# Kernel optimization log

Hardware: AMD Instinct MI355X
Metric: run time of the kernel (lower is better)

Reference implementation:

```python
import jax, jax.numpy as jnp
import numpy as np

B, T = 4096, 2048
CLIP = 1.0e5


def _hv(x):
    # smooth Heaviside: ~0 for x<0, ~1 for x>0
    return (jnp.tanh(5.0 * x) + 1.0) * 0.5


def setup_inputs() -> dict:
    key = jax.random.key(0)
    k1, _ = jax.random.split(key)
    # columns: prcp, tmean, dayl (all in [0,1) like normalized forcings)
    inputs = jax.random.uniform(k1, (B, T, 3), dtype=jnp.float32)
    # 15 scalar bucket parameters, all initialized to 0.5 as in build():
    # f, smax, qmax, ddf, tmin, tmax, Kc, SCmax, spmax, qpmax, kp, sgmax, qgmax, Kl, Kn
    theta = jnp.full((15,), 0.5, dtype=jnp.float32)
    return {"inputs": inputs, "theta": theta}


def _run(inputs, theta):
    f, smax, qmax, ddf, tmin, tmax, Kc, SCmax, spmax, qpmax, kp, sgmax, qgmax, Kl, Kn = [
        theta[i] for i in range(15)
    ]
    prcp = inputs[:, :, 0]   # [B,T]
    tmean = inputs[:, :, 1]
    dayl = inputs[:, :, 2]
    # Hamon-style PET computed once for the whole sequence
    pet = 29.8 * (dayl * 24.0) * 0.611 * jnp.exp(17.3 * tmean / (tmean + 237.3)) / (tmean + 273.2)

    # rescaled parameters (done once; constant over time)
    f_ = f / 10.0
    smax_ = smax * 1950.0
    qmax_ = qmax * 50.0
    ddf_ = ddf * 5.0
    tmin_ = tmin * -3.0
    tmax_ = tmax * 3.0
    Kc_ = Kc * 0.5
    SCmax_ = SCmax * 1.5
    spmax_ = spmax * 1950.0
    qpmax_ = qpmax * 40.0
    sgmax_ = sgmax * 1950.0
    qgmax_ = qgmax * 40.0
    Kl_ = Kl * 0.5
    Kn_ = Kn * 0.5
    Dc = 0.986 * 0.862

    def step(state, xt):
        s0, s1, s2, s3, s4 = [state[:, i] for i in range(5)]  # each [B]
        p, t, dl, pe = xt  # each [B]

        # canopy bucket
        day = _hv(dl - 0.5)
        night = _hv(0.5 - dl)
        scmax_t = day * SCmax_ * 2.0 + night * SCmax_ * 0.6
        lai_t = day * 0.478 + night * 0.15
        kc_t = day * Kc_ + night * Kc_ * 0.4
        pintc = (_hv(p - 0.1) * _hv(s0) * _hv(s0 - scmax_t) * p
                 + _hv(p - 0.1) * _hv(scmax_t - s0) * kc_t * Dc * lai_t)

        # rain/snow partition
        psnow = _hv(tmin_ - t) * p
        prain = _hv(t - tmin_) * p

        # snow bucket
        melt = _hv(t - tmax_) * _hv(s1) * jnp.minimum(s1, ddf_ * (t - tmax_))

        # preferential bucket
        qpref = (_hv(s2) * _hv(s2 - spmax_) * qpmax_
                 + _hv(s2) * _hv(spmax_ - s2) * kp * p * jnp.exp(-f_ * (spmax_ - s2)))

        # capillary (soil) bucket
        et = (_hv(s3) * _hv(s3 - smax_) * pe
              + _hv(s3) * _hv(smax_ - s3) * pe * (s3 / smax_))
        qsub = (_hv(s3) * _hv(s3 - smax_) * qmax_
                + _hv(s3) * _hv(smax_ - s3) * qmax_ * jnp.exp(-f_ * (smax_ - s3)))
        qout = _hv(s3) * _hv(s3 - smax_) * (s3 - smax_)

        # gravity bucket
        qslow = (_hv(s4) * _hv(s4 - sgmax_) * qgmax_
                 + _hv(s4) * _hv(sgmax_ - s4) * (p * Kl_ + p * p * Kn_) * jnp.exp(-f_ * (sgmax_ - s4)))

        ns0 = s0 + jnp.clip(pintc, -CLIP, CLIP)
        ns1 = s1 + jnp.clip(psnow - melt, -CLIP, CLIP)
        ns2 = s2 + jnp.clip(qpref, -CLIP, CLIP)
        ns3 = s3 + jnp.clip(prain + melt - et - qsub - qout, -CLIP, CLIP)
        ns4 = s4 + jnp.clip(qslow, -CLIP, CLIP)
        new_state = jnp.stack([ns0, ns1, ns2, ns3, ns4], axis=1)  # [B,5]
        return new_state, new_state

    init = jnp.zeros((inputs.shape[0], 5), dtype=inputs.dtype)
    xs = (prcp.T, tmean.T, dayl.T, pet.T)  # time-major [T,B]
    _, seq = jax.lax.scan(step, init, xs)  # seq: [T,B,5]
    return jnp.transpose(seq, (1, 0, 2))  # [B,T,5] state trajectories


def reference(inputs, theta):
    return _run(inputs, theta)
```

## Files before the change

kernel.cpp:

```cpp
#include <hip/hip_runtime.h>


#define NB 4096
#define NT 2048
#define CH0 16
#define K1 16
#define CH23 32
#define BT ((size_t)NB * (size_t)NT)

#define L2E10 14.4269504089f
#define L2E    1.44269504089f

__device__ __forceinline__ float rcpf(float x) { return __builtin_amdgcn_rcpf(x); }
__device__ __forceinline__ float ex2(float a)  { return __builtin_amdgcn_exp2f(a); }
__device__ __forceinline__ float ex2c(float a) { return __builtin_amdgcn_exp2f(fminf(a, 80.0f)); }
__device__ __forceinline__ float clip1e5(float x) {
    return __builtin_amdgcn_fmed3f(x, -100000.0f, 100000.0f);
}
__device__ __forceinline__ void pinbuf(const float* d, int n4) {
    const float4* v = (const float4*)d;
    #pragma unroll
    for (int i = 0; i < n4; ++i)
        asm volatile("" :: "v"(v[i].x), "v"(v[i].y), "v"(v[i].z), "v"(v[i].w));
}

__global__ __launch_bounds__(256)
void pre_kernel(const float* __restrict__ inp, const float* __restrict__ theta,
                float* __restrict__ out, float* __restrict__ wsp, int use_p0) {
    const float ddf_   = theta[3] * 5.0f;
    const float tmin_  = theta[4] * -3.0f;
    const float tmax_  = theta[5] * 3.0f;
    const float Kc_    = theta[6] * 0.5f;
    const float SCmax_ = theta[7] * 1.5f;
    const float KcDc  = Kc_ * 0.849932f;
    const float c_sn  = -L2E10 * tmin_;
    const float c_m   =  L2E10 * tmax_;
    const float c_dd  = -ddf_ * tmax_;
    const float c_sc1 =  L2E10 * SCmax_ * 1.4f;
    const float c_sc0 =  L2E10 * SCmax_ * 0.6f;

    const size_t k = (size_t)blockIdx.x * 256 + threadIdx.x;
    const float4* i4 = (const float4*)(inp + k * 12);
    const float4 A = i4[0], Bv = i4[1], C = i4[2];
    const float P[4] = {A.x, A.w, Bv.z, C.y};
    const float T[4] = {A.y, Bv.x, Bv.w, C.z};
    const float D[4] = {A.z, Bv.y, C.x, C.w};

    float4 pk1[4], pk0[4];
    float pp[4];
    #pragma unroll
    for (int j = 0; j < 4; ++j) {
        const float p = P[j], tm = T[j], dl = D[j];
        const float A1 = tm + 237.3f;
        const float A2 = tm + 273.2f;
        const float q  = rcpf(A1 * A2);
        const float pe = 436.98672f * dl * ex2(24.958624f * tm * (q * A2)) * (q * A1);
        const float psnow = rcpf(1.0f + ex2(fmaf(L2E10, tm, c_sn))) * p;
        const float dm  = 1.0f + ex2(fmaf(-L2E10, tm, c_m));
        const float mdd = fmaf(ddf_, tm, c_dd);
        pk1[j] = make_float4(pe, psnow, dm, mdd);
        pp[j] = p;
        if (use_p0) {
            const float day = rcpf(1.0f + ex2(fmaf(-L2E10, dl, 7.21347520f)));
            const float da  = 1.0f + ex2(fmaf(-L2E10, p, L2E));
            const float lai   = fmaf(0.328f, day, 0.15f);
            const float kcf   = fmaf(0.6f, day, 0.4f);
            const float kterm = KcDc * kcf * lai;
            const float zday  = fmaf(c_sc1, day, c_sc0);
            pk0[j] = make_float4(p, kterm, zday, da);
        }
    }
    float4* o1 = (float4*)out + k * 4;
    #pragma unroll
    for (int j = 0; j < 4; ++j) o1[j] = pk1[j];
    *(float4*)(out + 4 * BT + k * 4) = make_float4(pp[0], pp[1], pp[2], pp[3]);
    if (use_p0) {
        float4* o0 = (float4*)(wsp + 5 * BT) + k * 4;
        #pragma unroll
        for (int j = 0; j < 4; ++j) o0[j] = pk0[j];
    }
}

__global__ __launch_bounds__(64, 1)
void prnn_roles(const float* __restrict__ inp, const float* __restrict__ theta,
                float* __restrict__ out, float* __restrict__ wsp,
                int use_ws, int use_p0) {
    const int lane = threadIdx.x;
    const int role = blockIdx.x & 3;
    const int b = (blockIdx.x >> 2) * 64 + lane;

    const float f_     = theta[0] * 0.1f;
    const float smax_  = theta[1] * 1950.0f;
    const float qmax_  = theta[2] * 50.0f;
    const float ddf_   = theta[3] * 5.0f;
    const float tmin_  = theta[4] * -3.0f;
    const float tmax_  = theta[5] * 3.0f;
    const float Kc_    = theta[6] * 0.5f;
    const float SCmax_ = theta[7] * 1.5f;
    const float spmax_ = theta[8] * 1950.0f;
    const float qpmax_ = theta[9] * 40.0f;
    const float kp     = theta[10];
    const float sgmax_ = theta[11] * 1950.0f;
    const float qgmax_ = theta[12] * 40.0f;
    const float Kl_    = theta[13] * 0.5f;
    const float Kn_    = theta[14] * 0.5f;

    const float inv_smax = rcpf(smax_);
    const float KcDc  = Kc_ * 0.849932f;
    const float c_sn  = -L2E10 * tmin_;
    const float c_m   =  L2E10 * tmax_;
    const float c_dd  = -ddf_ * tmax_;
    const float c_sc1 =  L2E10 * SCmax_ * 1.4f;
    const float c_sc0 =  L2E10 * SCmax_ * 0.6f;
    const float c_2p  =  L2E10 * spmax_;
    const float c_3s  =  L2E10 * smax_;
    const float c_4s  =  L2E10 * sgmax_;
    const float fE    = f_ * L2E;
    const float c_E2  = -fE * spmax_;
    const float c_E3  = -fE * smax_;
    const float c_E4  = -fE * sgmax_;

    const float* ip = inp + (size_t)b * (NT * 3);
    float*       op = out + (size_t)b * (NT * 5);
    float* wbase = use_ws ? wsp : out;

    auto plane_storeN = [&](float* plane, const float* ob, int off, int n4) {
        float4* d = (float4*)(plane + (size_t)off);
        const float4* s = (const float4*)ob;
        #pragma unroll
        for (int i = 0; i < 8; ++i) { if (i < n4) d[i] = s[i]; }
    };

    if (role == 0) {
        float s0 = 0.f;
        float* w0 = wbase + 0 * BT + (size_t)b * NT;
        if (use_ws && use_p0) {
            const float4* PK = (const float4*)(wsp + 5 * BT) + (size_t)b * NT;
            float bA[CH0 * 4], bB[CH0 * 4];
            auto pf = [&](float* d, int c) {
                #pragma unroll
                for (int i = 0; i < CH0; ++i)
                    ((float4*)d)[i] = PK[(size_t)c * CH0 + i];
            };
            auto cw = [&](const float* d, int c) {
                float ob[CH0];
                #pragma unroll
                for (int i = 0; i < CH0; ++i) {
                    const float p     = d[i * 4 + 0];
                    const float kterm = d[i * 4 + 1];
                    const float zday  = d[i * 4 + 2];
                    const float da    = d[i * 4 + 3];
                    const float e0  = ex2(-L2E10 * s0);
                    const float esc = ex2(fmaf(-L2E10, s0, zday));
                    const float d0  = 1.0f + e0;
                    const float dsc = 1.0f + esc;
                    const float Rp  = rcpf(da * d0 * dsc);
                    const float pintc = Rp * fmaf(d0 * esc, kterm, p);
                    s0 += clip1e5(pintc);
                    ob[i] = s0;
                }
                plane_storeN(w0, ob, c * CH0, CH0 / 4);
            };
            pf(bA, 0);
            for (int c = 0; c < NT / CH0; c += 2) {
                pf(bB, c + 1);
                pinbuf(bA, CH0);
                cw(bA, c);
                if (c + 2 < NT / CH0) pf(bA, c + 2);
                pinbuf(bB, CH0);
                cw(bB, c + 1);
            }
        } else {
            float bA[CH0 * 3], bB[CH0 * 3];
            auto pf = [&](float* d, int c) {
                const float4* s = (const float4*)(ip + (size_t)c * (CH0 * 3));
                #pragma unroll
                for (int i = 0; i < (CH0 * 3) / 4; ++i) ((float4*)d)[i] = s[i];
            };
            auto cw = [&](const float* d, int c) {
                float ob[CH0];
                #pragma unroll
                for (int i = 0; i < CH0; ++i) {
                    const float p  = d[i * 3 + 0];
                    const float dl = d[i * 3 + 2];
                    const float day = rcpf(1.0f + ex2(fmaf(-L2E10, dl, 7.21347520f)));
                    const float da  = 1.0f + ex2(fmaf(-L2E10, p, L2E));
                    const float lai   = fmaf(0.328f, day, 0.15f);
                    const float kcf   = fmaf(0.6f, day, 0.4f);
                    const float kterm = KcDc * kcf * lai;
                    const float zday  = fmaf(c_sc1, day, c_sc0);
                    const float e0  = ex2(-L2E10 * s0);
                    const float esc = ex2(fmaf(-L2E10, s0, zday));
                    const float d0  = 1.0f + e0;
                    const float dsc = 1.0f + esc;
                    const float Rp  = rcpf(da * d0 * dsc);
                    const float pintc = Rp * fmaf(d0 * esc, kterm, p);
                    s0 += clip1e5(pintc);
                    ob[i] = s0;
                }
                if (use_ws) plane_storeN(w0, ob, c * CH0, CH0 / 4);
                else {
                    #pragma unroll
                    for (int i = 0; i < CH0; ++i) op[(c * CH0 + i) * 5 + 0] = ob[i];
                }
            };
            pf(bA, 0);
            for (int c = 0; c < NT / CH0; c += 2) {
                pf(bB, c + 1);
                pinbuf(bA, (CH0 * 3) / 4);
                cw(bA, c);
                if (c + 2 < NT / CH0) pf(bA, c + 2);
                pinbuf(bB, (CH0 * 3) / 4);
                cw(bB, c + 1);
            }
        }
    } else if (role == 1) {
        float s1 = 0.f, s3 = 0.f;
        float* w1 = wbase + 1 * BT + (size_t)b * NT;
        float* w3 = wbase + 3 * BT + (size_t)b * NT;
        if (use_ws) {
            const float4* PK = (const float4*)out + (size_t)b * NT;
            const float*  PP = out + 4 * BT + (size_t)b * NT;
            float kA[K1 * 4], kB[K1 * 4], pA[K1], pB[K1];
            float ob1[2 * K1], ob3[2 * K1];
            auto pf = [&](float* kd, float* pd, int c) {
                #pragma unroll
                for (int i = 0; i < K1; ++i)
                    ((float4*)kd)[i] = PK[(size_t)c * K1 + i];
                #pragma unroll
                for (int i = 0; i < K1 / 4; ++i)
                    ((float4*)pd)[i] = *(const float4*)(PP + (size_t)c * K1 + i * 4);
            };
            auto cw = [&](const float* kd, const float* pd, int half) {
                #pragma unroll
                for (int i = 0; i < K1; ++i) {
                    const float pe    = kd[i * 4 + 0];
                    const float psnow = kd[i * 4 + 1];
                    const float dm    = kd[i * 4 + 2];
                    const float mdd   = kd[i * 4 + 3];
                    const float prain = pd[i] - psnow;
                    const float e1 = ex2(-L2E10 * s1);
                    const float melt = rcpf(dm * (1.0f + e1)) * fminf(s1, mdd);
                    const float e3  = ex2(-L2E10 * s3);
                    const float e3s = ex2c(fmaf(-L2E10, s3, c_3s));
                    const float R3  = rcpf((1.0f + e3) * (1.0f + e3s));
                    const float E3  = ex2(fmaf(fE, s3, c_E3));
                    const float t_et = pe * fmaf(e3s * s3, inv_smax, 1.0f);
                    const float t_qs = qmax_ * fmaf(e3s, E3, 1.0f);
                    const float outflux = R3 * (t_et + t_qs + (s3 - smax_));
                    const float ds3 = prain + melt - outflux;
                    s1 += clip1e5(psnow - melt);
                    s3 += clip1e5(ds3);
                    ob1[half * K1 + i] = s1;
                    ob3[half * K1 + i] = s3;
                }
            };
            pf(kA, pA, 0);
            for (int c = 0; c < NT / K1; c += 2) {
                pf(kB, pB, c + 1);
                pinbuf(kA, K1); pinbuf(pA, K1 / 4);
                cw(kA, pA, 0);
                if (c + 2 < NT / K1) pf(kA, pA, c + 2);
                pinbuf(kB, K1); pinbuf(pB, K1 / 4);
                cw(kB, pB, 1);
                plane_storeN(w1, ob1, c * K1, (2 * K1) / 4);
                plane_storeN(w3, ob3, c * K1, (2 * K1) / 4);
            }
        } else {
            float bA[CH0 * 3], bB[CH0 * 3];
            auto pf = [&](float* d, int c) {
                const float4* s = (const float4*)(ip + (size_t)c * (CH0 * 3));
                #pragma unroll
                for (int i = 0; i < (CH0 * 3) / 4; ++i) ((float4*)d)[i] = s[i];
            };
            auto cw = [&](const float* d, int c) {
                #pragma unroll
                for (int i = 0; i < CH0; ++i) {
                    const float p  = d[i * 3 + 0];
                    const float tm = d[i * 3 + 1];
                    const float dl = d[i * 3 + 2];
                    const float A1 = tm + 237.3f;
                    const float A2 = tm + 273.2f;
                    const float qq = rcpf(A1 * A2);
                    const float pe = 436.98672f * dl * ex2(24.958624f * tm * (qq * A2)) * (qq * A1);
                    const float psnow = rcpf(1.0f + ex2(fmaf(L2E10, tm, c_sn))) * p;
                    const float dm = 1.0f + ex2(fmaf(-L2E10, tm, c_m));
                    const float prain = p - psnow;
                    const float e1 = ex2(-L2E10 * s1);
                    const float melt = rcpf(dm * (1.0f + e1))
                                       * fminf(s1, fmaf(ddf_, tm, c_dd));
                    const float e3  = ex2(-L2E10 * s3);
                    const float e3s = ex2c(fmaf(-L2E10, s3, c_3s));
                    const float R3  = rcpf((1.0f + e3) * (1.0f + e3s));
                    const float E3  = ex2(fmaf(fE, s3, c_E3));
                    const float t_et = pe * fmaf(e3s * s3, inv_smax, 1.0f);
                    const float t_qs = qmax_ * fmaf(e3s, E3, 1.0f);
                    const float outflux = R3 * (t_et + t_qs + (s3 - smax_));
                    const float ds3 = prain + melt - outflux;
                    s1 += clip1e5(psnow - melt);
                    s3 += clip1e5(ds3);
                    const int t = c * CH0 + i;
                    op[t * 5 + 1] = s1;
                    op[t * 5 + 3] = s3;
                }
            };
            pf(bA, 0);
            for (int c = 0; c < NT / CH0; c += 2) {
                pf(bB, c + 1);
                pinbuf(bA, (CH0 * 3) / 4);
                cw(bA, c);
                if (c + 2 < NT / CH0) pf(bA, c + 2);
                pinbuf(bB, (CH0 * 3) / 4);
                cw(bB, c + 1);
            }
        }
    } else if (role == 2) {
        float s2 = 0.f;
        float pA[CH23], pB[CH23];
        float* w2 = wbase + 2 * BT + (size_t)b * NT;
        const float* PP = out + 4 * BT + (size_t)b * NT;
        auto pf = [&](float* P, int c) {
            if (use_ws) {
                #pragma unroll
                for (int i = 0; i < CH23 / 4; ++i)
                    ((float4*)P)[i] = *(const float4*)(PP + (size_t)c * CH23 + i * 4);
            } else {
                #pragma unroll
                for (int i = 0; i < CH23; ++i) P[i] = ip[(c * CH23 + i) * 3 + 0];
            }
        };
        auto cw = [&](const float* P, int c) {
            float ob[CH23];
            #pragma unroll
            for (int i = 0; i < CH23; ++i) {
                const float p = P[i];
                const float e2  = ex2(-L2E10 * s2);
                const float e2p = ex2c(fmaf(-L2E10, s2, c_2p));
                const float R2  = rcpf((1.0f + e2) * (1.0f + e2p));
                const float E2  = ex2(fmaf(fE, s2, c_E2));
                const float qpref = R2 * fmaf(e2p * E2, kp * p, qpmax_);
                s2 += clip1e5(qpref);
                ob[i] = s2;
            }
            if (use_ws) plane_storeN(w2, ob, c * CH23, CH23 / 4);
            else {
                #pragma unroll
                for (int i = 0; i < CH23; ++i) op[(c * CH23 + i) * 5 + 2] = ob[i];
            }
        };
        pf(pA, 0);
        for (int c = 0; c < NT / CH23; c += 2) {
            pf(pB, c + 1);
            pinbuf(pA, CH23 / 4);
            cw(pA, c);
            if (c + 2 < NT / CH23) pf(pA, c + 2);
            pinbuf(pB, CH23 / 4);
            cw(pB, c + 1);
        }
    } else {
        float s4 = 0.f;
        float pA[CH23], pB[CH23];
        float* w4 = wbase + 4 * BT + (size_t)b * NT;
        const float* PP = out + 4 * BT + (size_t)b * NT;
        auto pf = [&](float* P, int c) {
            if (use_ws) {
                #pragma unroll
                for (int i = 0; i < CH23 / 4; ++i)
                    ((float4*)P)[i] = *(const float4*)(PP + (size_t)c * CH23 + i * 4);
            } else {
                #pragma unroll
                for (int i = 0; i < CH23; ++i) P[i] = ip[(c * CH23 + i) * 3 + 0];
            }
        };
        auto cw = [&](const float* P, int c) {
            float ob[CH23];
            #pragma unroll
            for (int i = 0; i < CH23; ++i) {
                const float p = P[i];
                const float e4  = ex2(-L2E10 * s4);
                const float e4s = ex2c(fmaf(-L2E10, s4, c_4s));
                const float R4  = rcpf((1.0f + e4) * (1.0f + e4s));
                const float E4  = ex2(fmaf(fE, s4, c_E4));
                const float pl  = p * fmaf(p, Kn_, Kl_);
                const float qslow = R4 * fmaf(e4s * E4, pl, qgmax_);
                s4 += clip1e5(qslow);
                ob[i] = s4;
            }
            if (use_ws) plane_storeN(w4, ob, c * CH23, CH23 / 4);
            else {
                #pragma unroll
                for (int i = 0; i < CH23; ++i) op[(c * CH23 + i) * 5 + 4] = ob[i];
            }
        };
        pf(pA, 0);
        for (int c = 0; c < NT / CH23; c += 2) {
            pf(pB, c + 1);
            pinbuf(pA, CH23 / 4);
            cw(pA, c);
            if (c + 2 < NT / CH23) pf(pA, c + 2);
            pinbuf(pB, CH23 / 4);
            cw(pB, c + 1);
        }
    }
}

__global__ __launch_bounds__(256)
void tx_kernel(const float* __restrict__ wsp, float* __restrict__ out) {
    const size_t idx = (size_t)blockIdx.x * 256 + threadIdx.x;
    const size_t b  = idx / (NT / 4);
    const size_t t0 = (idx % (NT / 4)) * 4;
    const float* base = wsp + b * NT + t0;
    const float4 v0 = *(const float4*)(base + 0 * BT);
    const float4 v1 = *(const float4*)(base + 1 * BT);
    const float4 v2 = *(const float4*)(base + 2 * BT);
    const float4 v3 = *(const float4*)(base + 3 * BT);
    const float4 v4 = *(const float4*)(base + 4 * BT);
    float4* o = (float4*)(out + (b * NT + t0) * 5);
    o[0] = make_float4(v0.x, v1.x, v2.x, v3.x);
    o[1] = make_float4(v4.x, v0.y, v1.y, v2.y);
    o[2] = make_float4(v3.y, v4.y, v0.z, v1.z);
    o[3] = make_float4(v2.z, v3.z, v4.z, v0.w);
    o[4] = make_float4(v1.w, v2.w, v3.w, v4.w);
}

extern "C" void kernel_launch(void* const* d_in, const int* in_sizes, int n_in,
                              void* d_out, int out_size, void* d_ws, size_t ws_size,
                              hipStream_t stream) {
    const float* inp   = (const float*)d_in[0];
    const float* theta = (const float*)d_in[1];
    float* out = (float*)d_out;
    float* wsp = (float*)d_ws;
    const int use_ws = (wsp != nullptr && ws_size >= 5 * sizeof(float) * BT) ? 1 : 0;
    const int use_p0 = (wsp != nullptr && ws_size >= 9 * sizeof(float) * BT) ? 1 : 0;
    if (use_ws)
        pre_kernel<<<(int)(BT / 4 / 256), 256, 0, stream>>>(inp, theta, out, wsp, use_p0);
    prnn_roles<<<4 * (NB / 64), 64, 0, stream>>>(inp, theta, out, wsp, use_ws, use_p0);
    if (use_ws)
        tx_kernel<<<(int)(BT / 4 / 256), 256, 0, stream>>>(wsp, out);
}
```

Before: 617.2 us.

## Split snow and soil recurrences of role 1 across two waves via LDS

Role 1 previously ran both the snow-bucket (s1) and soil-bucket (s3) recurrences serially in one wavefront. The block now has 128 threads. In role 1, wave 0 advances s1 and writes per-step melt into a double-buffered shared-memory array, and wave 1 reads the melt values to advance s3, synchronised every 16 steps with s_barrier. The aim is to shorten the serial dependent chain on the likely critical-path role, at the cost of barrier overhead and doubled block size; the other roles exit their second wave immediately.

```diff
diff --git a/kernel.cpp b/kernel.cpp
--- a/kernel.cpp
+++ b/kernel.cpp
@@ -5,6 +5,7 @@
 #define NT 2048
 #define CH0 16
 #define K1 16
+#define NCH1 (NT / K1)
 #define CH23 32
 #define BT ((size_t)NB * (size_t)NT)
 
@@ -81,13 +82,17 @@
     }
 }
 
-__global__ __launch_bounds__(64, 1)
+__global__ __launch_bounds__(128, 1)
 void prnn_roles(const float* __restrict__ inp, const float* __restrict__ theta,
                 float* __restrict__ out, float* __restrict__ wsp,
                 int use_ws, int use_p0) {
-    const int lane = threadIdx.x;
+    __shared__ float meltbuf[2][K1][64];
+    const int lane = threadIdx.x & 63;
+    const int wave = threadIdx.x >> 6;
     const int role = blockIdx.x & 3;
     const int b = (blockIdx.x >> 2) * 64 + lane;
+
+    if (role != 1 && wave != 0) return;
 
     const float f_     = theta[0] * 0.1f;
     const float smax_  = theta[1] * 1950.0f;
@@ -215,58 +220,95 @@
             }
         }
     } else if (role == 1) {
-        float s1 = 0.f, s3 = 0.f;
         float* w1 = wbase + 1 * BT + (size_t)b * NT;
         float* w3 = wbase + 3 * BT + (size_t)b * NT;
         if (use_ws) {
             const float4* PK = (const float4*)out + (size_t)b * NT;
             const float*  PP = out + 4 * BT + (size_t)b * NT;
-            float kA[K1 * 4], kB[K1 * 4], pA[K1], pB[K1];
-            float ob1[2 * K1], ob3[2 * K1];
-            auto pf = [&](float* kd, float* pd, int c) {
-                #pragma unroll
-                for (int i = 0; i < K1; ++i)
-                    ((float4*)kd)[i] = PK[(size_t)c * K1 + i];
-                #pragma unroll
-                for (int i = 0; i < K1 / 4; ++i)
-                    ((float4*)pd)[i] = *(const float4*)(PP + (size_t)c * K1 + i * 4);
-            };
-            auto cw = [&](const float* kd, const float* pd, int half) {
-                #pragma unroll
-                for (int i = 0; i < K1; ++i) {
-                    const float pe    = kd[i * 4 + 0];
-                    const float psnow = kd[i * 4 + 1];
-                    const float dm    = kd[i * 4 + 2];
-                    const float mdd   = kd[i * 4 + 3];
-                    const float prain = pd[i] - psnow;
-                    const float e1 = ex2(-L2E10 * s1);
-                    const float melt = rcpf(dm * (1.0f + e1)) * fminf(s1, mdd);
-                    const float e3  = ex2(-L2E10 * s3);
-                    const float e3s = ex2c(fmaf(-L2E10, s3, c_3s));
-                    const float R3  = rcpf((1.0f + e3) * (1.0f + e3s));
-                    const float E3  = ex2(fmaf(fE, s3, c_E3));
-                    const float t_et = pe * fmaf(e3s * s3, inv_smax, 1.0f);
-                    const float t_qs = qmax_ * fmaf(e3s, E3, 1.0f);
-                    const float outflux = R3 * (t_et + t_qs + (s3 - smax_));
-                    const float ds3 = prain + melt - outflux;
-                    s1 += clip1e5(psnow - melt);
-                    s3 += clip1e5(ds3);
-                    ob1[half * K1 + i] = s1;
-                    ob3[half * K1 + i] = s3;
-                }
-            };
-            pf(kA, pA, 0);
-            for (int c = 0; c < NT / K1; c += 2) {
-                pf(kB, pB, c + 1);
-                pinbuf(kA, K1); pinbuf(pA, K1 / 4);
-                cw(kA, pA, 0);
-                if (c + 2 < NT / K1) pf(kA, pA, c + 2);
-                pinbuf(kB, K1); pinbuf(pB, K1 / 4);
-                cw(kB, pB, 1);
-                plane_storeN(w1, ob1, c * K1, (2 * K1) / 4);
-                plane_storeN(w3, ob3, c * K1, (2 * K1) / 4);
+            if (wave == 0) {
+                float s1 = 0.f;
+                float kA[K1 * 4], kB[K1 * 4];
+                float ob1[2 * K1];
+                auto pf = [&](float* kd, int c) {
+                    #pragma unroll
+                    for (int i = 0; i < K1; ++i)
+                        ((float4*)kd)[i] = PK[(size_t)c * K1 + i];
+                };
+                auto cw = [&](const float* kd, int c, int half) {
+                    #pragma unroll
+                    for (int i = 0; i < K1; ++i) {
+                        const float psnow = kd[i * 4 + 1];
+                        const float dm    = kd[i * 4 + 2];
+                        const float mdd   = kd[i * 4 + 3];
+                        const float e1 = ex2(-L2E10 * s1);
+                        const float melt = rcpf(dm * (1.0f + e1)) * fminf(s1, mdd);
+                        meltbuf[c & 1][i][lane] = melt;
+                        s1 += clip1e5(psnow - melt);
+                        ob1[half * K1 + i] = s1;
+                    }
+                };
+                pf(kA, 0);
+                for (int c = 0; c < NCH1; c += 2) {
+                    pf(kB, c + 1);
+                    pinbuf(kA, K1);
+                    cw(kA, c, 0);
+                    asm volatile("s_waitcnt lgkmcnt(0)\n\ts_barrier" ::: "memory");
+                    if (c + 2 < NCH1) pf(kA, c + 2);
+                    pinbuf(kB, K1);
+                    cw(kB, c + 1, 1);
+                    asm volatile("s_waitcnt lgkmcnt(0)\n\ts_barrier" ::: "memory");
+                    plane_storeN(w1, ob1, c * K1, (2 * K1) / 4);
+                }
+            } else {
+                float s3 = 0.f;
+                float kA[K1 * 4], kB[K1 * 4], pA[K1], pB[K1];
+                float ob3[2 * K1];
+                auto pf = [&](float* kd, float* pd, int c) {
+                    #pragma unroll
+                    for (int i = 0; i < K1; ++i)
+                        ((float4*)kd)[i] = PK[(size_t)c * K1 + i];
+                    #pragma unroll
+                    for (int i = 0; i < K1 / 4; ++i)
+                        ((float4*)pd)[i] = *(const float4*)(PP + (size_t)c * K1 + i * 4);
+                };
+                auto cw = [&](const float* kd, const float* pd, int c, int half) {
+                    float ml[K1];
+                    #pragma unroll
+                    for (int i = 0; i < K1; ++i) ml[i] = meltbuf[c & 1][i][lane];
+                    #pragma unroll
+                    for (int i = 0; i < K1; ++i) {
+                        const float pe    = kd[i * 4 + 0];
+                        const float psnow = kd[i * 4 + 1];
+                        const float prain = pd[i] - psnow;
+                        const float melt  = ml[i];
+                        const float e3  = ex2(-L2E10 * s3);
+                        const float e3s = ex2c(fmaf(-L2E10, s3, c_3s));
+                        const float R3  = rcpf((1.0f + e3) * (1.0f + e3s));
+                        const float E3  = ex2(fmaf(fE, s3, c_E3));
+                        const float t_et = pe * fmaf(e3s * s3, inv_smax, 1.0f);
+                        const float t_qs = qmax_ * fmaf(e3s, E3, 1.0f);
+                        const float outflux = R3 * (t_et + t_qs + (s3 - smax_));
+                        const float ds3 = prain + melt - outflux;
+                        s3 += clip1e5(ds3);
+                        ob3[half * K1 + i] = s3;
+                    }
+                };
+                pf(kA, pA, 0);
+                for (int c = 0; c < NCH1; c += 2) {
+                    pf(kB, pB, c + 1);
+                    asm volatile("s_barrier" ::: "memory");
+                    pinbuf(kA, K1); pinbuf(pA, K1 / 4);
+                    cw(kA, pA, c, 0);
+                    asm volatile("s_barrier" ::: "memory");
+                    if (c + 2 < NCH1) pf(kA, pA, c + 2);
+                    pinbuf(kB, K1); pinbuf(pB, K1 / 4);
+                    cw(kB, pB, c + 1, 1);
+                    plane_storeN(w3, ob3, c * K1, (2 * K1) / 4);
+                }
             }
         } else {
+            if (wave != 0) return;
+            float s1 = 0.f, s3 = 0.f;
             float bA[CH0 * 3], bB[CH0 * 3];
             auto pf = [&](float* d, int c) {
                 const float4* s = (const float4*)(ip + (size_t)c * (CH0 * 3));
@@ -434,7 +476,7 @@
     const int use_p0 = (wsp != nullptr && ws_size >= 9 * sizeof(float) * BT) ? 1 : 0;
     if (use_ws)
         pre_kernel<<<(int)(BT / 4 / 256), 256, 0, stream>>>(inp, theta, out, wsp, use_p0);
-    prnn_roles<<<4 * (NB / 64), 64, 0, stream>>>(inp, theta, out, wsp, use_ws, use_p0);
+    prnn_roles<<<4 * (NB / 64), 128, 0, stream>>>(inp, theta, out, wsp, use_ws, use_p0);
     if (use_ws)
         tx_kernel<<<(int)(BT / 4 / 256), 256, 0, stream>>>(wsp, out);
 }
```

Result: slower. 652.2 us (+5.7%).

## Pack eight recurrence waves per block and widen transpose to eight timesteps

Applied to the files above, without the earlier changes.

The recurrent role kernel changes from 256 single-wave blocks to 32 blocks of 512 threads. Each block now holds eight waves that handle consecutive 64-batch groups, and the batch index is derived from the wave id. This puts several waves on each CU so they can hide each other's latency, but it uses far fewer CUs and lets waves on a SIMD compete for issue slots. The transpose kernel now handles eight timesteps per thread with wider loads and ten float4 stores, halving the grid size.

```diff
diff --git a/kernel.cpp b/kernel.cpp
--- a/kernel.cpp
+++ b/kernel.cpp
@@ -81,13 +81,14 @@
     }
 }
 
-__global__ __launch_bounds__(64, 1)
+__global__ __launch_bounds__(512, 1)
 void prnn_roles(const float* __restrict__ inp, const float* __restrict__ theta,
                 float* __restrict__ out, float* __restrict__ wsp,
                 int use_ws, int use_p0) {
-    const int lane = threadIdx.x;
+    const int lane = threadIdx.x & 63;
+    const int wave = threadIdx.x >> 6;
     const int role = blockIdx.x & 3;
-    const int b = (blockIdx.x >> 2) * 64 + lane;
+    const int b = ((blockIdx.x >> 2) * 8 + wave) * 64 + lane;
 
     const float f_     = theta[0] * 0.1f;
     const float smax_  = theta[1] * 1950.0f;
@@ -407,20 +408,24 @@
 __global__ __launch_bounds__(256)
 void tx_kernel(const float* __restrict__ wsp, float* __restrict__ out) {
     const size_t idx = (size_t)blockIdx.x * 256 + threadIdx.x;
-    const size_t b  = idx / (NT / 4);
-    const size_t t0 = (idx % (NT / 4)) * 4;
+    const size_t b  = idx / (NT / 8);
+    const size_t t0 = (idx % (NT / 8)) * 8;
     const float* base = wsp + b * NT + t0;
-    const float4 v0 = *(const float4*)(base + 0 * BT);
-    const float4 v1 = *(const float4*)(base + 1 * BT);
-    const float4 v2 = *(const float4*)(base + 2 * BT);
-    const float4 v3 = *(const float4*)(base + 3 * BT);
-    const float4 v4 = *(const float4*)(base + 4 * BT);
-    float4* o = (float4*)(out + (b * NT + t0) * 5);
-    o[0] = make_float4(v0.x, v1.x, v2.x, v3.x);
-    o[1] = make_float4(v4.x, v0.y, v1.y, v2.y);
-    o[2] = make_float4(v3.y, v4.y, v0.z, v1.z);
-    o[3] = make_float4(v2.z, v3.z, v4.z, v0.w);
-    o[4] = make_float4(v1.w, v2.w, v3.w, v4.w);
+    float v[5][8];
+    #pragma unroll
+    for (int s = 0; s < 5; ++s) {
+        *(float4*)&v[s][0] = *(const float4*)(base + s * BT);
+        *(float4*)&v[s][4] = *(const float4*)(base + s * BT + 4);
+    }
+    float o[40];
+    #pragma unroll
+    for (int t = 0; t < 8; ++t)
+        #pragma unroll
+        for (int s = 0; s < 5; ++s) o[t * 5 + s] = v[s][t];
+    float4* d = (float4*)(out + (b * NT + t0) * 5);
+    const float4* sv = (const float4*)o;
+    #pragma unroll
+    for (int i = 0; i < 10; ++i) d[i] = sv[i];
 }
 
 extern "C" void kernel_launch(void* const* d_in, const int* in_sizes, int n_in,
@@ -434,7 +439,7 @@
     const int use_p0 = (wsp != nullptr && ws_size >= 9 * sizeof(float) * BT) ? 1 : 0;
     if (use_ws)
         pre_kernel<<<(int)(BT / 4 / 256), 256, 0, stream>>>(inp, theta, out, wsp, use_p0);
-    prnn_roles<<<4 * (NB / 64), 64, 0, stream>>>(inp, theta, out, wsp, use_ws, use_p0);
+    prnn_roles<<<32, 512, 0, stream>>>(inp, theta, out, wsp, use_ws, use_p0);
     if (use_ws)
-        tx_kernel<<<(int)(BT / 4 / 256), 256, 0, stream>>>(wsp, out);
-}
+        tx_kernel<<<(int)(BT / 8 / 256), 256, 0, stream>>>(wsp, out);
+}
```

New measurement: 1.543 ms. +150.0%, slower.
